# Kernel optimization log

Measured on AMD Instinct MI355X. Metric: run time of the kernel, lower is better.

The kernel has to match this reference:

```python
import jax, jax.numpy as jnp
import numpy as np

NODE_DIM = 2
EMB_DIM = 128
SEQ_LEN = 5000
BATCH = 64


def _cyclic_positional_encoding(n_position, emb_dim, mean_pooling=True):
    """Faithful numpy port of EmbeddingNet.Cyclic_Positional_Encoding (init-time constant)."""
    Td_set = np.linspace(np.power(n_position, 1 / (emb_dim // 2)), n_position, emb_dim // 2, dtype='int')
    x = np.zeros((n_position, emb_dim))
    for i in range(emb_dim):
        Td = Td_set[i // 3 * 3 + 1] if i // 3 * 3 + 1 < emb_dim // 2 else Td_set[-1]
        fai = 0 if i <= emb_dim // 2 else 2 * np.pi * ((-i + emb_dim // 2) / (emb_dim // 2))
        longer = np.arange(0, np.ceil(n_position / Td) * Td, 0.01)
        idx = np.linspace(0, len(longer), n_position, dtype='int', endpoint=False)
        base = 2 * np.pi / Td * np.abs(np.mod(longer, 2 * Td) - Td) + fai
        x[:, i] = (np.cos(base) if i % 2 == 1 else np.sin(base))[idx]
    pat = x.astype(np.float32)
    ar = np.arange(n_position)
    shifts = [-2, -1, 0, 1, 2] if mean_pooling else [0]
    acc = np.zeros_like(pat)
    for s in shifts:
        acc += pat[(ar + s + n_position) % n_position]
    pat = acc / float(len(shifts)) - pat.mean(0)
    return jnp.asarray(pat, dtype=jnp.float32)


def setup_inputs() -> dict:
    key = jax.random.key(0)
    kx, kw, ks = jax.random.split(key, 3)
    x = jax.random.normal(kx, (BATCH, SEQ_LEN, NODE_DIM), dtype=jnp.float32)
    stdv = 1.0 / np.sqrt(NODE_DIM)
    W = jax.random.uniform(kw, (EMB_DIM, NODE_DIM), dtype=jnp.float32, minval=-stdv, maxval=stdv)
    pattern = _cyclic_positional_encoding(SEQ_LEN, EMB_DIM)  # [S, D]

    # solutions must be a single-cycle successor permutation over SEQ_LEN nodes
    def make_cycle(k):
        p = jax.random.permutation(k, SEQ_LEN)
        return jnp.zeros(SEQ_LEN, jnp.int32).at[p].set(jnp.roll(p, -1).astype(jnp.int32))

    solutions = jax.vmap(make_cycle)(jax.random.split(ks, BATCH))  # [B, S] int32
    return {"x": x, "W": W, "pattern": pattern, "solutions": solutions}


def reference(x, W, pattern, solutions):
    B, S = solutions.shape
    # pointer-chase: pre=0; visited_time[solutions[pre]] = i+1; pre = solutions[pre]
    def step(pre, _):
        nxt = jnp.take_along_axis(solutions, pre[:, None], axis=1)[:, 0]
        return nxt, nxt

    _, order = jax.lax.scan(step, jnp.zeros(B, dtype=solutions.dtype), None, length=S)
    order = order.T  # [B, S]: node visited at step i
    visited_time = jnp.zeros((B, S), jnp.int32).at[
        jnp.arange(B)[:, None], order
    ].set(jnp.arange(1, S + 1, dtype=jnp.int32)[None, :])
    idx = visited_time % S  # [B, S]
    PFEs = pattern[idx]  # gather -> [B, S, D]
    NFEs = jnp.einsum('bsn,dn->bsd', x, W)  # Linear(node_dim->emb, no bias)
    return NFEs, PFEs, visited_time
```

## Files before the change

kernel.cpp:

```cpp
#include <hip/hip_runtime.h>

#define SEQ 5000
#define BATCH 64
#define DIM 128

#define TPB1 1024
#define TPB2 512
#define ROWS_PER_ITER (TPB2 / 32)
#define EMIT_BLOCKS 2048

typedef float f32x4 __attribute__((ext_vector_type(4)));

__global__ __launch_bounds__(TPB1) void rank_kernel(
    const int* __restrict__ sol,
    float* __restrict__ vt_out) {
    __shared__ unsigned buf[2][SEQ];
    const int b = blockIdx.x;
    const int* sp = sol + b * SEQ;

    for (int i = threadIdx.x; i < SEQ; i += TPB1) {
        unsigned nx = (unsigned)sp[i];
        if (nx >= SEQ) nx = 0;
        buf[0][i] = (i == 0) ? 0u : ((1u << 16) | nx);
    }
    __syncthreads();
    int cur = 0;
#pragma unroll 1
    for (int it = 0; it < 13; ++it) {
        for (int i = threadIdx.x; i < SEQ; i += TPB1) {
            unsigned w  = buf[cur][i];
            unsigned w2 = buf[cur][w & 0xFFFFu];
            buf[cur ^ 1][i] = (w & 0xFFFF0000u) + w2;
        }
        __syncthreads();
        cur ^= 1;
    }
    for (int i = threadIdx.x; i < SEQ; i += TPB1) {
        int vt = SEQ - (int)(buf[cur][i] >> 16);
        vt_out[(size_t)b * SEQ + i] = (float)vt;
    }
}

__global__ __launch_bounds__(TPB2) void emit_kernel(
    const float2* __restrict__ x,
    const f32x4* __restrict__ W,
    const f32x4* __restrict__ pat,
    const float* __restrict__ vt_in,
    float* __restrict__ out) {
    const size_t NFE = (size_t)BATCH * SEQ * DIM;
    f32x4* nfe4 = (f32x4*)out;
    f32x4* pfe4 = (f32x4*)(out + NFE);

    const int c = threadIdx.x & 31;
    f32x4 wa = W[c * 2 + 0];
    f32x4 wb = W[c * 2 + 1];

    const size_t TOT = (size_t)BATCH * SEQ;
    for (size_t r = (size_t)blockIdx.x * ROWS_PER_ITER + (threadIdx.x >> 5);
         r < TOT; r += (size_t)gridDim.x * ROWS_PER_ITER) {
        int vt = (int)vt_in[r];
        int i = (vt >= SEQ) ? 0 : vt;
        if ((unsigned)i >= SEQ) i = 0;

        float2 xv = x[r];
        f32x4 nv;
        nv.x = fmaf(xv.x, wa.x, xv.y * wa.y);
        nv.y = fmaf(xv.x, wa.z, xv.y * wa.w);
        nv.z = fmaf(xv.x, wb.x, xv.y * wb.y);
        nv.w = fmaf(xv.x, wb.z, xv.y * wb.w);
        __builtin_nontemporal_store(nv, &nfe4[r * 32 + c]);

        f32x4 pv = pat[(size_t)i * 32 + c];
        __builtin_nontemporal_store(pv, &pfe4[r * 32 + c]);
    }
}

extern "C" void kernel_launch(void* const* d_in, const int* in_sizes, int n_in,
                              void* d_out, int out_size, void* d_ws, size_t ws_size,
                              hipStream_t stream) {
    const void* xp = d_in[0];
    const void* wp = d_in[1];
    const void* pp = d_in[2];
    const void* sp = d_in[3];
    {
        const void* big[2] = {nullptr, nullptr};
        int nbig = 0;
        const void *w_ = nullptr, *s_ = nullptr;
        for (int i = 0; i < n_in; ++i) {
            if (in_sizes[i] == DIM * 2) w_ = d_in[i];
            else if (in_sizes[i] == BATCH * SEQ) s_ = d_in[i];
            else if (in_sizes[i] == SEQ * DIM && nbig < 2) big[nbig++] = d_in[i];
        }
        if (w_ && s_ && nbig == 2) { wp = w_; sp = s_; xp = big[0]; pp = big[1]; }
    }

    const size_t NFE = (size_t)BATCH * SEQ * DIM;
    float* vt_out = (float*)d_out + 2 * NFE;

    rank_kernel<<<BATCH, TPB1, 0, stream>>>((const int*)sp, vt_out);
    emit_kernel<<<EMIT_BLOCKS, TPB2, 0, stream>>>(
        (const float2*)xp, (const f32x4*)wp, (const f32x4*)pp,
        (const float*)vt_out, (float*)d_out);
}
```

Before: 351.5 us.

## Overlap NFE linear projection with pointer-chase ranking in one launch

The NFE projection does not depend on visited_time, so it now runs in extra blocks of the rank kernel while 64 blocks do the pointer-jumping rank computation. The second kernel only gathers PFE rows from the pattern. This hides the mostly idle, latency-bound ranking phase behind NFE write traffic. The cost is that the NFE blocks take 1024 threads each and sit beside blocks holding large shared-memory buffers, which may affect scheduling.

After: 334.8 us, median of 2. 1.05x faster.

```diff
diff --git a/kernel.cpp b/kernel.cpp
--- a/kernel.cpp
+++ b/kernel.cpp
@@ -5,71 +5,84 @@
 #define DIM 128
 
 #define TPB1 1024
+#define RANK_BLOCKS BATCH
+#define NFE_BLOCKS 960
 #define TPB2 512
-#define ROWS_PER_ITER (TPB2 / 32)
-#define EMIT_BLOCKS 2048
+#define PFE_BLOCKS 2048
 
 typedef float f32x4 __attribute__((ext_vector_type(4)));
 
-__global__ __launch_bounds__(TPB1) void rank_kernel(
+__global__ __launch_bounds__(TPB1) void rank_nfe_kernel(
+    const float2* __restrict__ x,
+    const f32x4* __restrict__ W,
     const int* __restrict__ sol,
-    float* __restrict__ vt_out) {
+    float* __restrict__ out) {
     __shared__ unsigned buf[2][SEQ];
-    const int b = blockIdx.x;
-    const int* sp = sol + b * SEQ;
+    const size_t NFE = (size_t)BATCH * SEQ * DIM;
 
-    for (int i = threadIdx.x; i < SEQ; i += TPB1) {
-        unsigned nx = (unsigned)sp[i];
-        if (nx >= SEQ) nx = 0;
-        buf[0][i] = (i == 0) ? 0u : ((1u << 16) | nx);
-    }
-    __syncthreads();
-    int cur = 0;
-#pragma unroll 1
-    for (int it = 0; it < 13; ++it) {
+    if (blockIdx.x < RANK_BLOCKS) {
+        const int b = blockIdx.x;
+        const int* sp = sol + b * SEQ;
+        float* vt_out = out + 2 * NFE;
+
         for (int i = threadIdx.x; i < SEQ; i += TPB1) {
-            unsigned w  = buf[cur][i];
-            unsigned w2 = buf[cur][w & 0xFFFFu];
-            buf[cur ^ 1][i] = (w & 0xFFFF0000u) + w2;
+            unsigned nx = (unsigned)sp[i];
+            if (nx >= SEQ) nx = 0;
+            buf[0][i] = (i == 0) ? 0u : ((1u << 16) | nx);
         }
         __syncthreads();
-        cur ^= 1;
-    }
-    for (int i = threadIdx.x; i < SEQ; i += TPB1) {
-        int vt = SEQ - (int)(buf[cur][i] >> 16);
-        vt_out[(size_t)b * SEQ + i] = (float)vt;
+        int cur = 0;
+#pragma unroll 1
+        for (int it = 0; it < 13; ++it) {
+            for (int i = threadIdx.x; i < SEQ; i += TPB1) {
+                unsigned w  = buf[cur][i];
+                unsigned w2 = buf[cur][w & 0xFFFFu];
+                buf[cur ^ 1][i] = (w & 0xFFFF0000u) + w2;
+            }
+            __syncthreads();
+            cur ^= 1;
+        }
+        for (int i = threadIdx.x; i < SEQ; i += TPB1) {
+            int vt = SEQ - (int)(buf[cur][i] >> 16);
+            vt_out[(size_t)b * SEQ + i] = (float)vt;
+        }
+    } else {
+        f32x4* nfe4 = (f32x4*)out;
+        const int c = threadIdx.x & 31;
+        f32x4 wa = W[c * 2 + 0];
+        f32x4 wb = W[c * 2 + 1];
+
+        const size_t TOT = (size_t)BATCH * SEQ;
+        const int ROWS = TPB1 / 32;
+        for (size_t r = (size_t)(blockIdx.x - RANK_BLOCKS) * ROWS +
+                        (threadIdx.x >> 5);
+             r < TOT; r += (size_t)NFE_BLOCKS * ROWS) {
+            float2 xv = x[r];
+            f32x4 nv;
+            nv.x = fmaf(xv.x, wa.x, xv.y * wa.y);
+            nv.y = fmaf(xv.x, wa.z, xv.y * wa.w);
+            nv.z = fmaf(xv.x, wb.x, xv.y * wb.y);
+            nv.w = fmaf(xv.x, wb.z, xv.y * wb.w);
+            __builtin_nontemporal_store(nv, &nfe4[r * 32 + c]);
+        }
     }
 }
 
-__global__ __launch_bounds__(TPB2) void emit_kernel(
-    const float2* __restrict__ x,
-    const f32x4* __restrict__ W,
+__global__ __launch_bounds__(TPB2) void pfe_kernel(
     const f32x4* __restrict__ pat,
     const float* __restrict__ vt_in,
     float* __restrict__ out) {
     const size_t NFE = (size_t)BATCH * SEQ * DIM;
-    f32x4* nfe4 = (f32x4*)out;
     f32x4* pfe4 = (f32x4*)(out + NFE);
-
     const int c = threadIdx.x & 31;
-    f32x4 wa = W[c * 2 + 0];
-    f32x4 wb = W[c * 2 + 1];
 
     const size_t TOT = (size_t)BATCH * SEQ;
-    for (size_t r = (size_t)blockIdx.x * ROWS_PER_ITER + (threadIdx.x >> 5);
-         r < TOT; r += (size_t)gridDim.x * ROWS_PER_ITER) {
+    const int ROWS = TPB2 / 32;
+    for (size_t r = (size_t)blockIdx.x * ROWS + (threadIdx.x >> 5);
+         r < TOT; r += (size_t)PFE_BLOCKS * ROWS) {
         int vt = (int)vt_in[r];
         int i = (vt >= SEQ) ? 0 : vt;
         if ((unsigned)i >= SEQ) i = 0;
-
-        float2 xv = x[r];
-        f32x4 nv;
-        nv.x = fmaf(xv.x, wa.x, xv.y * wa.y);
-        nv.y = fmaf(xv.x, wa.z, xv.y * wa.w);
-        nv.z = fmaf(xv.x, wb.x, xv.y * wb.y);
-        nv.w = fmaf(xv.x, wb.z, xv.y * wb.w);
-        __builtin_nontemporal_store(nv, &nfe4[r * 32 + c]);
-
         f32x4 pv = pat[(size_t)i * 32 + c];
         __builtin_nontemporal_store(pv, &pfe4[r * 32 + c]);
     }
@@ -95,10 +108,10 @@
     }
 
     const size_t NFE = (size_t)BATCH * SEQ * DIM;
-    float* vt_out = (float*)d_out + 2 * NFE;
+    float* vt_region = (float*)d_out + 2 * NFE;
 
-    rank_kernel<<<BATCH, TPB1, 0, stream>>>((const int*)sp, vt_out);
-    emit_kernel<<<EMIT_BLOCKS, TPB2, 0, stream>>>(
-        (const float2*)xp, (const f32x4*)wp, (const f32x4*)pp,
-        (const float*)vt_out, (float*)d_out);
+    rank_nfe_kernel<<<RANK_BLOCKS + NFE_BLOCKS, TPB1, 0, stream>>>(
+        (const float2*)xp, (const f32x4*)wp, (const int*)sp, (float*)d_out);
+    pfe_kernel<<<PFE_BLOCKS, TPB2, 0, stream>>>(
+        (const f32x4*)pp, (const float*)vt_region, (float*)d_out);
 }
```
